# Kernel tuning notes

Measured on AMD Instinct MI355X. Metric: run time of the kernel, lower is better.

The kernel has to match this reference:

```python
import jax, jax.numpy as jnp
import numpy as np

BETA = 0.25


def setup_inputs() -> dict:
    key = jax.random.key(0)
    k1, k2 = jax.random.split(key)
    inp = jax.random.normal(k1, (8, 64, 64, 64), dtype=jnp.float32)   # [B,C,H,W]
    book = jax.random.normal(k2, (8192, 64), dtype=jnp.float32)       # [K,D], D==C
    return {"input": inp, "book": book}


def reference(input, book):
    # Faithful translation of the original forward (including its quirks:
    # the cross term is summed to a SCALAR, and z_q is viewed back into
    # input.shape (NCHW) before permute(0,3,1,2) -> [B,W,C,H]).
    B, C, H, W = input.shape
    D = book.shape[1]  # == C
    z = jnp.transpose(input, (0, 2, 3, 1)).reshape(-1, D)          # [N, D]
    # scalar cross term: sum_{n,k} z_n . e_k == (sum_n z_n) . (sum_k e_k)
    cross = jnp.dot(jnp.sum(z, axis=0), jnp.sum(book, axis=0))
    d = (jnp.sum(z * z, axis=1, keepdims=True)                     # [N,1]
         + jnp.sum(book * book, axis=1)                            # [K]  -> broadcast [N,K]
         - 2.0 * cross)
    idx = jnp.argmin(d, axis=1)                                     # [N]
    z_q = book[idx].reshape(input.shape)                            # raw reshape to [B,C,H,W]
    loss = (jnp.mean((jax.lax.stop_gradient(z_q) - input) ** 2)
            + BETA * jnp.mean((z_q - jax.lax.stop_gradient(input)) ** 2))
    z_q = jnp.transpose(z_q, (0, 3, 1, 2))                          # [B,W,C,H] as in source
    return (z_q, idx, loss)
```

## Files before the change

kernel.cpp:

```cpp
#include <hip/hip_runtime.h>


#define NTOT    2097152
#define NIDX    32768
#define K_ROWS  8192
#define K1_BLK  512
#define K2_BLK  512
#define K2_ITER 4


__global__ __launch_bounds__(256) void k1_argmin(const float* __restrict__ book,
                                                 unsigned long long* __restrict__ ws_keys) {
    const int t   = threadIdx.x;
    const int rIn = t >> 4;
    const int c4  = t & 15;
    const int row = blockIdx.x * 16 + rIn;

    const float4 v = ((const float4*)book)[row * 16 + c4];
    float s = v.x * v.x + v.y * v.y + v.z * v.z + v.w * v.w;
    s += __shfl_down(s, 8, 16);
    s += __shfl_down(s, 4, 16);
    s += __shfl_down(s, 2, 16);
    s += __shfl_down(s, 1, 16);

    __shared__ unsigned long long keys[16];
    if (c4 == 0) {
        keys[rIn] = ((unsigned long long)__float_as_uint(s) << 32)
                  | (unsigned int)row;
    }
    __syncthreads();
    if (t == 0) {
        unsigned long long k = keys[0];
        #pragma unroll
        for (int i = 1; i < 16; ++i) k = keys[i] < k ? keys[i] : k;
        ws_keys[blockIdx.x] = k;
    }
}

__global__ __launch_bounds__(256) void k2_main(const float* __restrict__ in,
                                               const float* __restrict__ book,
                                               float* __restrict__ out,
                                               const unsigned long long* __restrict__ ws_keys,
                                               float* __restrict__ ws_part) {
    const int lane = threadIdx.x & 63, wid = threadIdx.x >> 6;

    __shared__ unsigned long long skey;
    if (wid == 0) {
        unsigned long long key = ~0ULL;
        #pragma unroll
        for (int j = 0; j < K1_BLK / 64; ++j) {
            unsigned long long o = ws_keys[lane + j * 64];
            key = o < key ? o : key;
        }
        #pragma unroll
        for (int off = 32; off > 0; off >>= 1) {
            unsigned long long o = __shfl_down(key, off, 64);
            key = o < key ? o : key;
        }
        if (lane == 0) skey = key;
    }
    __syncthreads();
    const int kmin = (int)(skey & 0xFFFFFFFFu);
    const float* __restrict__ e = book + kmin * 64;

    const int tid = blockIdx.x * 256 + threadIdx.x;

    if (tid < NIDX / 4) {
        const float kf = (float)kmin;
        ((float4*)(out + NTOT))[tid] = make_float4(kf, kf, kf, kf);
    }

    float part = 0.f;
    #pragma unroll
    for (int it = 0; it < K2_ITER; ++it) {
        const int i = tid + it * (K2_BLK * 256);
        const float ev = e[(i >> 10) & 63];
        ((float4*)out)[i] = make_float4(ev, ev, ev, ev);
        const float4 z  = ((const float4*)in)[i];
        const float4 ef = ((const float4*)e)[i & 15];
        const float d0 = z.x - ef.x, d1 = z.y - ef.y;
        const float d2 = z.z - ef.z, d3 = z.w - ef.w;
        part += d0 * d0 + d1 * d1 + d2 * d2 + d3 * d3;
    }
    #pragma unroll
    for (int off = 32; off > 0; off >>= 1) part += __shfl_down(part, off, 64);

    __shared__ float sp[4];
    if (lane == 0) sp[wid] = part;
    __syncthreads();
    if (threadIdx.x == 0)
        ws_part[blockIdx.x] = sp[0] + sp[1] + sp[2] + sp[3];
}

__global__ __launch_bounds__(64) void k3_loss(const float* __restrict__ ws_part,
                                              float* __restrict__ out) {
    float s = 0.f;
    #pragma unroll
    for (int j = 0; j < K2_BLK / 64; ++j) s += ws_part[threadIdx.x + j * 64];
    #pragma unroll
    for (int off = 32; off > 0; off >>= 1) s += __shfl_down(s, off, 64);
    if (threadIdx.x == 0)
        out[NTOT + NIDX] = s * (1.25f / (float)NTOT);
}

extern "C" void kernel_launch(void* const* d_in, const int* in_sizes, int n_in,
                              void* d_out, int out_size, void* d_ws, size_t ws_size,
                              hipStream_t stream) {
    const float* in   = (const float*)d_in[0];
    const float* book = (const float*)d_in[1];
    float* out = (float*)d_out;

    unsigned long long* ws_keys = (unsigned long long*)d_ws;
    float*              ws_part = (float*)((char*)d_ws + 4096);

    k1_argmin<<<K1_BLK, 256, 0, stream>>>(book, ws_keys);
    k2_main<<<K2_BLK, 256, 0, stream>>>(in, book, out, ws_keys, ws_part);
    k3_loss<<<1, 64, 0, stream>>>(ws_part, out);
}
```

Measured before the change: 67.53 us.

## Expand loss algebraically and fold input stats into argmin kernel, drop loss kernel

The input read and its statistics (per-column sums and the total sum of squares) move into the first kernel alongside the codebook norms. The loss is then computed in closed form as T - 2*e·s + N*|e|^2, so the write kernel no longer reads the input at all. The last block of the write kernel produces the final loss, which removes the third launch. The cost is a serial reduction over 512x16 float4 partials in one block, and that block assumes it sees the partials from the previous launch. Reordering the floating-point sums may change rounding slightly.

```diff
diff --git a/kernel.cpp b/kernel.cpp
--- a/kernel.cpp
+++ b/kernel.cpp
@@ -3,33 +3,67 @@
 
 #define NTOT    2097152
 #define NIDX    32768
-#define K_ROWS  8192
-#define K1_BLK  512
-#define K2_BLK  512
-#define K2_ITER 4
+#define NBLK    512
 
 
-__global__ __launch_bounds__(256) void k1_argmin(const float* __restrict__ book,
-                                                 unsigned long long* __restrict__ ws_keys) {
-    const int t   = threadIdx.x;
-    const int rIn = t >> 4;
-    const int c4  = t & 15;
-    const int row = blockIdx.x * 16 + rIn;
-
-    const float4 v = ((const float4*)book)[row * 16 + c4];
-    float s = v.x * v.x + v.y * v.y + v.z * v.z + v.w * v.w;
-    s += __shfl_down(s, 8, 16);
-    s += __shfl_down(s, 4, 16);
-    s += __shfl_down(s, 2, 16);
-    s += __shfl_down(s, 1, 16);
+__global__ __launch_bounds__(256) void kA_stats(const float* __restrict__ in,
+                                                const float* __restrict__ book,
+                                                unsigned long long* __restrict__ ws_keys,
+                                                float* __restrict__ ws_T,
+                                                float4* __restrict__ ws_sw) {
+    const int t    = threadIdx.x;
+    const int lane = t & 63, wid = t >> 6;
 
     __shared__ unsigned long long keys[16];
-    if (c4 == 0) {
-        keys[rIn] = ((unsigned long long)__float_as_uint(s) << 32)
-                  | (unsigned int)row;
+    __shared__ float4 swv[4][16];
+    __shared__ float  twv[4];
+
+    {
+        const int rIn = t >> 4, c4 = t & 15;
+        const int row = blockIdx.x * 16 + rIn;
+        const float4 v = ((const float4*)book)[row * 16 + c4];
+        float s = v.x * v.x + v.y * v.y + v.z * v.z + v.w * v.w;
+        s += __shfl_down(s, 8, 16);
+        s += __shfl_down(s, 4, 16);
+        s += __shfl_down(s, 2, 16);
+        s += __shfl_down(s, 1, 16);
+        if (c4 == 0) {
+            keys[rIn] = ((unsigned long long)__float_as_uint(s) << 32)
+                      | (unsigned int)row;
+        }
     }
+
+    const int tid = blockIdx.x * 256 + t;
+    float4 cs = make_float4(0.f, 0.f, 0.f, 0.f);
+    float  tp = 0.f;
+    #pragma unroll
+    for (int it = 0; it < 4; ++it) {
+        const float4 z = ((const float4*)in)[tid + it * (NBLK * 256)];
+        cs.x += z.x; cs.y += z.y; cs.z += z.z; cs.w += z.w;
+        tp += z.x * z.x + z.y * z.y + z.z * z.z + z.w * z.w;
+    }
+    #pragma unroll
+    for (int off = 32; off >= 16; off >>= 1) {
+        cs.x += __shfl_down(cs.x, off, 64);
+        cs.y += __shfl_down(cs.y, off, 64);
+        cs.z += __shfl_down(cs.z, off, 64);
+        cs.w += __shfl_down(cs.w, off, 64);
+    }
+    #pragma unroll
+    for (int off = 32; off > 0; off >>= 1) tp += __shfl_down(tp, off, 64);
+
+    if (lane < 16) swv[wid][lane] = cs;
+    if (lane == 0) twv[wid] = tp;
     __syncthreads();
+
+    if (t < 16) {
+        const float4 a = swv[0][t], b = swv[1][t], c = swv[2][t], d = swv[3][t];
+        ws_sw[blockIdx.x * 16 + t] =
+            make_float4(a.x + b.x + c.x + d.x, a.y + b.y + c.y + d.y,
+                        a.z + b.z + c.z + d.z, a.w + b.w + c.w + d.w);
+    }
     if (t == 0) {
+        ws_T[blockIdx.x] = twv[0] + twv[1] + twv[2] + twv[3];
         unsigned long long k = keys[0];
         #pragma unroll
         for (int i = 1; i < 16; ++i) k = keys[i] < k ? keys[i] : k;
@@ -37,24 +71,24 @@
     }
 }
 
-__global__ __launch_bounds__(256) void k2_main(const float* __restrict__ in,
-                                               const float* __restrict__ book,
-                                               float* __restrict__ out,
-                                               const unsigned long long* __restrict__ ws_keys,
-                                               float* __restrict__ ws_part) {
+__global__ __launch_bounds__(256) void kB_write(const float* __restrict__ book,
+                                                float* __restrict__ out,
+                                                const unsigned long long* __restrict__ ws_keys,
+                                                const float* __restrict__ ws_T,
+                                                const float* __restrict__ ws_sw_f) {
     const int lane = threadIdx.x & 63, wid = threadIdx.x >> 6;
 
     __shared__ unsigned long long skey;
     if (wid == 0) {
         unsigned long long key = ~0ULL;
         #pragma unroll
-        for (int j = 0; j < K1_BLK / 64; ++j) {
-            unsigned long long o = ws_keys[lane + j * 64];
+        for (int j = 0; j < NBLK / 64; ++j) {
+            const unsigned long long o = ws_keys[lane + j * 64];
             key = o < key ? o : key;
         }
         #pragma unroll
         for (int off = 32; off > 0; off >>= 1) {
-            unsigned long long o = __shfl_down(key, off, 64);
+            const unsigned long long o = __shfl_down(key, off, 64);
             key = o < key ? o : key;
         }
         if (lane == 0) skey = key;
@@ -70,37 +104,43 @@
         ((float4*)(out + NTOT))[tid] = make_float4(kf, kf, kf, kf);
     }
 
-    float part = 0.f;
     #pragma unroll
-    for (int it = 0; it < K2_ITER; ++it) {
-        const int i = tid + it * (K2_BLK * 256);
+    for (int it = 0; it < 4; ++it) {
+        const int i = tid + it * (NBLK * 256);
         const float ev = e[(i >> 10) & 63];
         ((float4*)out)[i] = make_float4(ev, ev, ev, ev);
-        const float4 z  = ((const float4*)in)[i];
-        const float4 ef = ((const float4*)e)[i & 15];
-        const float d0 = z.x - ef.x, d1 = z.y - ef.y;
-        const float d2 = z.z - ef.z, d3 = z.w - ef.w;
-        part += d0 * d0 + d1 * d1 + d2 * d2 + d3 * d3;
     }
-    #pragma unroll
-    for (int off = 32; off > 0; off >>= 1) part += __shfl_down(part, off, 64);
 
-    __shared__ float sp[4];
-    if (lane == 0) sp[wid] = part;
-    __syncthreads();
-    if (threadIdx.x == 0)
-        ws_part[blockIdx.x] = sp[0] + sp[1] + sp[2] + sp[3];
-}
-
-__global__ __launch_bounds__(64) void k3_loss(const float* __restrict__ ws_part,
-                                              float* __restrict__ out) {
-    float s = 0.f;
-    #pragma unroll
-    for (int j = 0; j < K2_BLK / 64; ++j) s += ws_part[threadIdx.x + j * 64];
-    #pragma unroll
-    for (int off = 32; off > 0; off >>= 1) s += __shfl_down(s, off, 64);
-    if (threadIdx.x == 0)
-        out[NTOT + NIDX] = s * (1.25f / (float)NTOT);
+    if (blockIdx.x == NBLK - 1) {
+        __shared__ float swv[4][64];
+        __shared__ float tpv[4];
+        float s = 0.f;
+        for (int j = 0; j < NBLK / 4; ++j)
+            s += ws_sw_f[(wid * (NBLK / 4) + j) * 64 + lane];
+        swv[wid][lane] = s;
+        float tq = ws_T[threadIdx.x] + ws_T[threadIdx.x + 256];
+        #pragma unroll
+        for (int off = 32; off > 0; off >>= 1) tq += __shfl_down(tq, off, 64);
+        if (lane == 0) tpv[wid] = tq;
+        __syncthreads();
+        if (threadIdx.x < 64) {
+            const int w = threadIdx.x;
+            const float sw = swv[0][w] + swv[1][w] + swv[2][w] + swv[3][w];
+            const float ew = e[w];
+            float cross = ew * sw;
+            float e2    = ew * ew;
+            #pragma unroll
+            for (int off = 32; off > 0; off >>= 1) {
+                cross += __shfl_down(cross, off, 64);
+                e2    += __shfl_down(e2,    off, 64);
+            }
+            if (w == 0) {
+                const float T = tpv[0] + tpv[1] + tpv[2] + tpv[3];
+                const float lsum = T - 2.f * cross + (float)(NTOT / 64) * e2;
+                out[NTOT + NIDX] = lsum * (1.25f / (float)NTOT);
+            }
+        }
+    }
 }
 
 extern "C" void kernel_launch(void* const* d_in, const int* in_sizes, int n_in,
@@ -111,9 +151,10 @@
     float* out = (float*)d_out;
 
     unsigned long long* ws_keys = (unsigned long long*)d_ws;
-    float*              ws_part = (float*)((char*)d_ws + 4096);
+    float*              ws_T    = (float*)((char*)d_ws + 4096);
+    float4*             ws_sw   = (float4*)((char*)d_ws + 8192);
+    const float*        ws_sw_f = (const float*)((char*)d_ws + 8192);
 
-    k1_argmin<<<K1_BLK, 256, 0, stream>>>(book, ws_keys);
-    k2_main<<<K2_BLK, 256, 0, stream>>>(in, book, out, ws_keys, ws_part);
-    k3_loss<<<1, 64, 0, stream>>>(ws_part, out);
+    kA_stats<<<NBLK, 256, 0, stream>>>(in, book, ws_keys, ws_T, ws_sw);
+    kB_write<<<NBLK, 256, 0, stream>>>(book, out, ws_keys, ws_T, ws_sw_f);
 }
```

Measured after the change: 69.86 us. 1.03x slower.
